# Optimization experiments

Measured on AMD Instinct MI355X. Metric: run time of the kernel, lower is better.

Reference implementation:

```python
import jax, jax.numpy as jnp
import numpy as np

N_NODES = 100000
N_EDGES = 1000000
IN_DIM = 64
HID_DIM = 64


def _gcn_conv(x, W, b, rows, cols, deg_inv_sqrt):
    # x: [N, Fin] -> [N, Fout]; rows/cols already include self-loops
    xw = x @ W                                   # [N, Fout]
    norm = deg_inv_sqrt[rows] * deg_inv_sqrt[cols]  # [E+N]
    msg = xw[cols] * norm[:, None]               # gather + scale, [E+N, Fout]
    out = jax.ops.segment_sum(msg, rows, num_segments=x.shape[0])  # scatter-add
    return out + b


def _prelu(x, a):
    return jnp.where(x >= 0, x, a * x)


def _encode(x, edge_index, perm, W1, b1, prelu_a, W2, b2):
    N = x.shape[0]
    loops = jnp.arange(N, dtype=edge_index.dtype)
    rows = jnp.concatenate([edge_index[0], loops])
    cols = jnp.concatenate([edge_index[1], loops])
    deg = jax.ops.segment_sum(jnp.ones_like(rows, dtype=x.dtype), rows, num_segments=N)
    dis = jnp.where(deg > 0, jax.lax.rsqrt(deg), 0.0)

    def enc(feat):
        h = _gcn_conv(feat, W1, b1, rows, cols, dis)
        h = _prelu(h, prelu_a)
        return _gcn_conv(h, W2, b2, rows, cols, dis)

    positive = enc(x)
    negative = enc(x[perm])  # corruption: row permutation of features
    summary = jax.nn.sigmoid(positive.mean(axis=0))
    return positive, negative, summary


def setup_inputs() -> dict:
    key = jax.random.key(0)
    kx, ke, kp, k1, k2 = jax.random.split(key, 5)
    x = jax.random.normal(kx, (N_NODES, IN_DIM), dtype=jnp.float32)
    edge_index = jax.random.randint(ke, (2, N_EDGES), 0, N_NODES, dtype=jnp.int32)
    perm = jax.random.permutation(kp, N_NODES).astype(jnp.int32)
    s1 = 1.0 / np.sqrt(IN_DIM)
    s2 = 1.0 / np.sqrt(HID_DIM)
    W1 = jax.random.uniform(k1, (IN_DIM, HID_DIM), jnp.float32, -s1, s1)
    b1 = jnp.zeros((HID_DIM,), jnp.float32)
    W2 = jax.random.uniform(k2, (HID_DIM, HID_DIM), jnp.float32, -s2, s2)
    b2 = jnp.zeros((HID_DIM,), jnp.float32)
    prelu_a = jnp.float32(0.25)
    return {"x": x, "edge_index": edge_index, "perm": perm,
            "W1": W1, "b1": b1, "prelu_a": prelu_a, "W2": W2, "b2": b2}


def reference(x, edge_index, perm, W1, b1, prelu_a, W2, b2):
    return _encode(x, edge_index, perm, W1, b1, prelu_a, W2, b2)
```

## Files before the change

kernel.cpp:

```cpp
#include <hip/hip_runtime.h>
#include <hip/hip_fp16.h>
#include <math.h>

namespace {

constexpr int NN = 100000;
constexpr int NE = 1000000;
constexpr int D  = 64;

constexpr int RPB_LOG = 8;
constexpr int RPB = 1 << RPB_LOG;
constexpr int NBUK = (NN + RPB - 1) >> RPB_LOG;
constexpr int CAP = 4096;
constexpr int TILE = 8192;
constexpr int NTILES = (NE + TILE - 1) / TILE;
constexpr int EPT = TILE / 512;
constexpr int G1B = (NN / 16 + 7) / 8;

using ushort_t = unsigned short;
typedef __attribute__((ext_vector_type(8))) short short8;
typedef __attribute__((ext_vector_type(4))) float f32x4;

union FragU { uint4 v; short8 s; };

__device__ inline void split2(float f0, float f1, unsigned int& hi, unsigned int& lo) {
    unsigned int u0 = __float_as_uint(f0);
    unsigned int u1 = __float_as_uint(f1);
    hi = (u0 >> 16) | (u1 & 0xffff0000u);
    float l0 = f0 - __uint_as_float(u0 & 0xffff0000u);
    float l1 = f1 - __uint_as_float(u1 & 0xffff0000u);
    lo = (__float_as_uint(l0) >> 16) | (__float_as_uint(l1) & 0xffff0000u);
}

__device__ inline unsigned int packh(float a, float b) {
    union { __half2 h; unsigned int u; } cv;
    cv.h = __float22half2_rn(make_float2(a, b));
    return cv.u;
}

__device__ inline float2 h2f(unsigned int v) {
    union { unsigned int u; __half2 h; } cv;
    cv.u = v;
    return __half22float2(cv.h);
}

__device__ inline void build_wfrags(const float* __restrict__ W, int lane,
                                    FragU (&whi)[4][2], FragU (&wlo)[4][2]) {
#pragma unroll
    for (int ft = 0; ft < 4; ++ft) {
#pragma unroll
        for (int kt = 0; kt < 2; ++kt) {
            int m  = ft * 16 + (lane & 15);
            int k0 = kt * 32 + (lane >> 4) * 8;
            unsigned int hi0, lo0, hi1, lo1, hi2, lo2, hi3, lo3;
            split2(W[(k0 + 0) * 64 + m], W[(k0 + 1) * 64 + m], hi0, lo0);
            split2(W[(k0 + 2) * 64 + m], W[(k0 + 3) * 64 + m], hi1, lo1);
            split2(W[(k0 + 4) * 64 + m], W[(k0 + 5) * 64 + m], hi2, lo2);
            split2(W[(k0 + 6) * 64 + m], W[(k0 + 7) * 64 + m], hi3, lo3);
            whi[ft][kt].v = make_uint4(hi0, hi1, hi2, hi3);
            wlo[ft][kt].v = make_uint4(lo0, lo1, lo2, lo3);
        }
    }
}

__global__ void pre_k(const int* __restrict__ rows, const int* __restrict__ cols,
                      int* __restrict__ bcount, unsigned int* __restrict__ binned, int e,
                      const float* __restrict__ W1, const float* __restrict__ W2,
                      uint4* __restrict__ fb,
                      const float* __restrict__ x, const int* __restrict__ perm,
                      ushort_t* __restrict__ tPN) {
    __shared__ int hist[NBUK];
    __shared__ int gbase[NBUK];
    __shared__ int lofs[NBUK];
    int bid = blockIdx.x;

    if (bid > NTILES) {
        int lane  = threadIdx.x & 63;
        int wtile = (bid - NTILES - 1) * 8 + (threadIdx.x >> 6);
        if (wtile * 16 >= NN) return;
        int node = wtile * 16 + (lane & 15);
        int kg   = lane >> 4;

        FragU whi[4][2];
        FragU wlo[4][2];
        build_wfrags(W1, lane, whi, wlo);

        const float4* xr = (const float4*)x;
        size_t rbase = (size_t)node * 16 + (size_t)(kg * 2);
        int pnode = perm[node];
        size_t pbase = (size_t)pnode * 16 + (size_t)(kg * 2);
        f32x4 accP[4];
        f32x4 accN[4];
#pragma unroll
        for (int ft = 0; ft < 4; ++ft) {
            accP[ft] = f32x4{0.f, 0.f, 0.f, 0.f};
            accN[ft] = f32x4{0.f, 0.f, 0.f, 0.f};
        }
#pragma unroll
        for (int kt = 0; kt < 2; ++kt) {
            float4 a0 = xr[rbase + kt * 8];
            float4 a1 = xr[rbase + kt * 8 + 1];
            float4 g0 = xr[pbase + kt * 8];
            float4 g1 = xr[pbase + kt * 8 + 1];
            unsigned int h0, l0, h1, l1, h2, l2, h3, l3;
            split2(a0.x, a0.y, h0, l0);
            split2(a0.z, a0.w, h1, l1);
            split2(a1.x, a1.y, h2, l2);
            split2(a1.z, a1.w, h3, l3);
            FragU xhiP, xloP;
            xhiP.v = make_uint4(h0, h1, h2, h3);
            xloP.v = make_uint4(l0, l1, l2, l3);
            split2(g0.x, g0.y, h0, l0);
            split2(g0.z, g0.w, h1, l1);
            split2(g1.x, g1.y, h2, l2);
            split2(g1.z, g1.w, h3, l3);
            FragU xhiN, xloN;
            xhiN.v = make_uint4(h0, h1, h2, h3);
            xloN.v = make_uint4(l0, l1, l2, l3);
#pragma unroll
            for (int ft = 0; ft < 4; ++ft) {
                accP[ft] = __builtin_amdgcn_mfma_f32_16x16x32_bf16(whi[ft][kt].s, xhiP.s, accP[ft], 0, 0, 0);
                accP[ft] = __builtin_amdgcn_mfma_f32_16x16x32_bf16(whi[ft][kt].s, xloP.s, accP[ft], 0, 0, 0);
                accP[ft] = __builtin_amdgcn_mfma_f32_16x16x32_bf16(wlo[ft][kt].s, xhiP.s, accP[ft], 0, 0, 0);
                accN[ft] = __builtin_amdgcn_mfma_f32_16x16x32_bf16(whi[ft][kt].s, xhiN.s, accN[ft], 0, 0, 0);
                accN[ft] = __builtin_amdgcn_mfma_f32_16x16x32_bf16(whi[ft][kt].s, xloN.s, accN[ft], 0, 0, 0);
                accN[ft] = __builtin_amdgcn_mfma_f32_16x16x32_bf16(wlo[ft][kt].s, xhiN.s, accN[ft], 0, 0, 0);
            }
        }
        int fo = kg * 4;
        ushort_t* p = tPN + (size_t)node * 128;
#pragma unroll
        for (int ft = 0; ft < 4; ++ft) {
            uint2 up = make_uint2(packh(accP[ft][0], accP[ft][1]),
                                  packh(accP[ft][2], accP[ft][3]));
            *(uint2*)(p + ft * 16 + fo) = up;
            uint2 un = make_uint2(packh(accN[ft][0], accN[ft][1]),
                                  packh(accN[ft][2], accN[ft][3]));
            *(uint2*)(p + 64 + ft * 16 + fo) = un;
        }
        return;
    }

    if (bid == NTILES) {
        int lane = threadIdx.x;
        if (lane < 64) {
            for (int ft = 0; ft < 4; ++ft) {
                for (int kt = 0; kt < 2; ++kt) {
                    int m  = ft * 16 + (lane & 15);
                    int k0 = kt * 32 + (lane >> 4) * 8;
                    unsigned int hi0, lo0, hi1, lo1, hi2, lo2, hi3, lo3;
                    split2(W2[(k0 + 0) * 64 + m], W2[(k0 + 1) * 64 + m], hi0, lo0);
                    split2(W2[(k0 + 2) * 64 + m], W2[(k0 + 3) * 64 + m], hi1, lo1);
                    split2(W2[(k0 + 4) * 64 + m], W2[(k0 + 5) * 64 + m], hi2, lo2);
                    split2(W2[(k0 + 6) * 64 + m], W2[(k0 + 7) * 64 + m], hi3, lo3);
                    fb[((ft * 2 + kt) * 2 + 0) * 64 + lane] = make_uint4(hi0, hi1, hi2, hi3);
                    fb[((ft * 2 + kt) * 2 + 1) * 64 + lane] = make_uint4(lo0, lo1, lo2, lo3);
                }
            }
        }
        return;
    }

    int base = bid * TILE;
    for (int i = threadIdx.x; i < NBUK; i += blockDim.x) {
        hist[i] = 0;
        lofs[i] = 0;
    }
    __syncthreads();
    int r[EPT];
    int c[EPT];
    int bk[EPT];
#pragma unroll
    for (int j = 0; j < EPT; ++j) {
        int i = base + j * 512 + (int)threadIdx.x;
        if (i < e) {
            r[j] = rows[i];
            c[j] = cols[i];
            bk[j] = r[j] >> RPB_LOG;
            atomicAdd(&hist[bk[j]], 1);
        } else {
            bk[j] = -1;
        }
    }
    __syncthreads();
    for (int b = threadIdx.x; b < NBUK; b += blockDim.x) {
        int h = hist[b];
        gbase[b] = h ? atomicAdd(&bcount[b], h) : 0;
    }
    __syncthreads();
#pragma unroll
    for (int j = 0; j < EPT; ++j) {
        if (bk[j] >= 0) {
            int l = gbase[bk[j]] + atomicAdd(&lofs[bk[j]], 1);
            if (l < CAP) {
                unsigned int v = ((unsigned int)(r[j] & (RPB - 1)) << 17) | (unsigned int)c[j];
                binned[(size_t)bk[j] * CAP + l] = v;
            }
        }
    }
}

__global__ void bucket_sort_k(const unsigned int* __restrict__ binned,
                              const int* __restrict__ bcount,
                              int* __restrict__ scols, int* __restrict__ rowstart,
                              int* __restrict__ deg, float* __restrict__ dis) {
    __shared__ int lcur[RPB];
    __shared__ int srs[RPB];
    __shared__ int wsum[8];
    __shared__ int redpart[8];
    __shared__ int sbase;
    int b = blockIdx.x;
    int row0 = b << RPB_LOG;
    int nrows = min(RPB, NN - row0);
    int cnt = bcount[b];
    const unsigned int* src = binned + (size_t)b * CAP;
    int tid = threadIdx.x;
    int lane = tid & 63;
    int wid = tid >> 6;

    int bv = (tid < NBUK && tid < b) ? bcount[tid] : 0;
    int bs = bv;
#pragma unroll
    for (int off = 1; off < 64; off <<= 1) {
        bs += __shfl_xor(bs, off, 64);
    }
    if (lane == 0) redpart[wid] = bs;
    __syncthreads();
    if (tid == 0) {
        int t = 0;
        for (int w = 0; w < 8; ++w) t += redpart[w];
        sbase = t;
    }
    if (tid < RPB) {
        lcur[tid] = 0;
    }
    __syncthreads();
    int bb = sbase;

    for (int i = tid; i < cnt; i += blockDim.x) {
        atomicAdd(&lcur[src[i] >> 17], 1);
    }
    __syncthreads();
    int d = (tid < nrows) ? lcur[tid] : 0;
    int inc = d;
#pragma unroll
    for (int off = 1; off < 64; off <<= 1) {
        int t = __shfl_up(inc, off);
        if (lane >= off) inc += t;
    }
    if (lane == 63) wsum[wid] = inc;
    __syncthreads();
    int wpre = 0;
    for (int w = 0; w < wid; ++w) wpre += wsum[w];
    int gstart = bb + wpre + inc - d;
    if (tid < nrows) {
        rowstart[row0 + tid] = gstart;
        deg[row0 + tid] = d;
        dis[row0 + tid] = rsqrtf((float)(d + 1));
    }
    __syncthreads();
    if (tid < RPB) {
        srs[tid] = gstart;
        lcur[tid] = 0;
    }
    __syncthreads();
    for (int i = tid; i < cnt; i += blockDim.x) {
        unsigned int v = src[i];
        int rl = (int)(v >> 17);
        int pos = srs[rl] + atomicAdd(&lcur[rl], 1);
        scols[pos] = (int)(v & 0x1FFFFu);
    }
}

__global__ void agg_gemm_k(const ushort_t* __restrict__ tIn, ushort_t* __restrict__ tOut,
                           const float* __restrict__ dis,
                           const int* __restrict__ rowstart, const int* __restrict__ deg,
                           const int* __restrict__ scols,
                           const float* __restrict__ bias, const float* __restrict__ prelu_a,
                           const uint4* __restrict__ wf) {
    __shared__ float Hs[2][16][68];
    int tid = threadIdx.x;
    int lane = tid & 63;
    int wv = tid >> 6;
    int row0 = blockIdx.x * 16;
    int hl = lane & 31;
    int half = lane >> 5;
    size_t lofs = (size_t)(half * 64 + hl * 2);
    float aPr = *prelu_a;

    for (int rr = 0; rr < 4; ++rr) {
        int r = row0 + wv * 4 + rr;
        int rs   = __builtin_amdgcn_readfirstlane(r);
        int base = __builtin_amdgcn_readfirstlane(rowstart[rs]);
        int dg   = __builtin_amdgcn_readfirstlane(deg[rs]);
        float dr = dis[rs];
        unsigned int sv = *(const unsigned int*)(tIn + (size_t)rs * 128 + lofs);
        float2 fs = h2f(sv);
        float a0 = dr * fs.x;
        float a1 = dr * fs.y;
        int j = 0;
        for (; j + 4 <= dg; j += 4) {
            int c0 = scols[base + j];
            int c1 = scols[base + j + 1];
            int c2 = scols[base + j + 2];
            int c3 = scols[base + j + 3];
            float d0 = dis[c0];
            float d1 = dis[c1];
            float d2 = dis[c2];
            float d3 = dis[c3];
            unsigned int v0 = *(const unsigned int*)(tIn + (size_t)c0 * 128 + lofs);
            unsigned int v1 = *(const unsigned int*)(tIn + (size_t)c1 * 128 + lofs);
            unsigned int v2 = *(const unsigned int*)(tIn + (size_t)c2 * 128 + lofs);
            unsigned int v3 = *(const unsigned int*)(tIn + (size_t)c3 * 128 + lofs);
            float2 f0 = h2f(v0);
            float2 f1 = h2f(v1);
            float2 f2 = h2f(v2);
            float2 f3 = h2f(v3);
            a0 = fmaf(d0, f0.x, a0);
            a1 = fmaf(d0, f0.y, a1);
            a0 = fmaf(d1, f1.x, a0);
            a1 = fmaf(d1, f1.y, a1);
            a0 = fmaf(d2, f2.x, a0);
            a1 = fmaf(d2, f2.y, a1);
            a0 = fmaf(d3, f3.x, a0);
            a1 = fmaf(d3, f3.y, a1);
        }
        for (; j < dg; ++j) {
            int c = scols[base + j];
            float dc = dis[c];
            unsigned int v = *(const unsigned int*)(tIn + (size_t)c * 128 + lofs);
            float2 f = h2f(v);
            a0 = fmaf(dc, f.x, a0);
            a1 = fmaf(dc, f.y, a1);
        }
        float2 bv = *(const float2*)(bias + 2 * hl);
        float v0 = fmaf(dr, a0, bv.x);
        float v1 = fmaf(dr, a1, bv.y);
        v0 = v0 >= 0.f ? v0 : aPr * v0;
        v1 = v1 >= 0.f ? v1 : aPr * v1;
        int rl = wv * 4 + rr;
        Hs[half][rl][2 * hl]     = v0;
        Hs[half][rl][2 * hl + 1] = v1;
    }
    __syncthreads();

    int kg = lane >> 4;
    int nd = lane & 15;
    int hsel = wv >> 1;
    int ftb = (wv & 1) * 2;
    FragU whi[2][2];
    FragU wlo[2][2];
#pragma unroll
    for (int f2 = 0; f2 < 2; ++f2) {
#pragma unroll
        for (int kt = 0; kt < 2; ++kt) {
            whi[f2][kt].v = wf[(((ftb + f2) * 2 + kt) * 2 + 0) * 64 + lane];
            wlo[f2][kt].v = wf[(((ftb + f2) * 2 + kt) * 2 + 1) * 64 + lane];
        }
    }
    f32x4 acc[2];
    acc[0] = f32x4{0.f, 0.f, 0.f, 0.f};
    acc[1] = f32x4{0.f, 0.f, 0.f, 0.f};
#pragma unroll
    for (int kt = 0; kt < 2; ++kt) {
        float4 a0 = *(const float4*)&Hs[hsel][nd][kt * 32 + kg * 8];
        float4 a1 = *(const float4*)&Hs[hsel][nd][kt * 32 + kg * 8 + 4];
        unsigned int h0, l0, h1, l1, h2, l2, h3, l3;
        split2(a0.x, a0.y, h0, l0);
        split2(a0.z, a0.w, h1, l1);
        split2(a1.x, a1.y, h2, l2);
        split2(a1.z, a1.w, h3, l3);
        FragU xhi, xlo;
        xhi.v = make_uint4(h0, h1, h2, h3);
        xlo.v = make_uint4(l0, l1, l2, l3);
#pragma unroll
        for (int f2 = 0; f2 < 2; ++f2) {
            acc[f2] = __builtin_amdgcn_mfma_f32_16x16x32_bf16(whi[f2][kt].s, xhi.s, acc[f2], 0, 0, 0);
            acc[f2] = __builtin_amdgcn_mfma_f32_16x16x32_bf16(whi[f2][kt].s, xlo.s, acc[f2], 0, 0, 0);
            acc[f2] = __builtin_amdgcn_mfma_f32_16x16x32_bf16(wlo[f2][kt].s, xhi.s, acc[f2], 0, 0, 0);
        }
    }
    float s = dis[row0 + nd];
    ushort_t* p = tOut + (size_t)(row0 + nd) * 128 + hsel * 64;
    int fo = kg * 4;
#pragma unroll
    for (int f2 = 0; f2 < 2; ++f2) {
        uint2 u = make_uint2(packh(s * acc[f2][0], s * acc[f2][1]),
                             packh(s * acc[f2][2], s * acc[f2][3]));
        *(uint2*)(p + (ftb + f2) * 16 + fo) = u;
    }
}

__global__ void agg_dual_k(const ushort_t* __restrict__ tPN,
                           float* __restrict__ dstP, float* __restrict__ dstN,
                           const float* __restrict__ dis,
                           const int* __restrict__ rowstart, const int* __restrict__ deg,
                           const int* __restrict__ scols,
                           const float* __restrict__ bias, int n) {
    int lane = threadIdx.x & 63;
    int hl = lane & 31;
    int half = lane >> 5;
    int r = blockIdx.x * (blockDim.x >> 6) + (threadIdx.x >> 6);
    if (r >= n) return;
    int rs   = __builtin_amdgcn_readfirstlane(r);
    int base = __builtin_amdgcn_readfirstlane(rowstart[rs]);
    int dg   = __builtin_amdgcn_readfirstlane(deg[rs]);
    float dr = dis[rs];
    size_t lofs = (size_t)(half * 64 + hl * 2);
    unsigned int sv = *(const unsigned int*)(tPN + (size_t)rs * 128 + lofs);
    float2 fs = h2f(sv);
    float a0 = fs.x;
    float a1 = fs.y;
    int j = 0;
    for (; j + 4 <= dg; j += 4) {
        int c0 = scols[base + j];
        int c1 = scols[base + j + 1];
        int c2 = scols[base + j + 2];
        int c3 = scols[base + j + 3];
        unsigned int v0 = *(const unsigned int*)(tPN + (size_t)c0 * 128 + lofs);
        unsigned int v1 = *(const unsigned int*)(tPN + (size_t)c1 * 128 + lofs);
        unsigned int v2 = *(const unsigned int*)(tPN + (size_t)c2 * 128 + lofs);
        unsigned int v3 = *(const unsigned int*)(tPN + (size_t)c3 * 128 + lofs);
        float2 f0 = h2f(v0);
        float2 f1 = h2f(v1);
        float2 f2 = h2f(v2);
        float2 f3 = h2f(v3);
        a0 += f0.x + f1.x + f2.x + f3.x;
        a1 += f0.y + f1.y + f2.y + f3.y;
    }
    for (; j < dg; ++j) {
        int c = scols[base + j];
        unsigned int v = *(const unsigned int*)(tPN + (size_t)c * 128 + lofs);
        float2 f = h2f(v);
        a0 += f.x;
        a1 += f.y;
    }
    float2 bv = *(const float2*)(bias + 2 * hl);
    float v0 = fmaf(dr, a0, bv.x);
    float v1 = fmaf(dr, a1, bv.y);
    float* dst = half ? dstN : dstP;
    *(float2*)(dst + (size_t)rs * D + 2 * hl) = float2{v0, v1};
}

__global__ void summary_partial_k(const float* __restrict__ pos, float* __restrict__ acc, int n) {
    __shared__ float red[4][64];
    int lane = threadIdx.x & 63;
    int wv = threadIdx.x >> 6;
    int wave = (blockIdx.x * blockDim.x + threadIdx.x) >> 6;
    int nw = (gridDim.x * blockDim.x) >> 6;
    float s0 = 0.f, s1 = 0.f, s2 = 0.f, s3 = 0.f;
    int r = wave;
    for (; r + 3 * nw < n; r += 4 * nw) {
        s0 += pos[(size_t)r * D + lane];
        s1 += pos[(size_t)(r + nw) * D + lane];
        s2 += pos[(size_t)(r + 2 * nw) * D + lane];
        s3 += pos[(size_t)(r + 3 * nw) * D + lane];
    }
    for (; r < n; r += nw) {
        s0 += pos[(size_t)r * D + lane];
    }
    red[wv][lane] = (s0 + s1) + (s2 + s3);
    __syncthreads();
    if (wv == 0) {
        float t = (red[0][lane] + red[1][lane]) + (red[2][lane] + red[3][lane]);
        atomicAdd(&acc[lane], t);
    }
}

__global__ void summary_final_k(const float* __restrict__ acc, float* __restrict__ out, int n) {
    int f = threadIdx.x;
    if (f < D) {
        float m = acc[f] / (float)n;
        out[f] = 1.f / (1.f + expf(-m));
    }
}

}

extern "C" void kernel_launch(void* const* d_in, const int* in_sizes, int n_in,
                              void* d_out, int out_size, void* d_ws, size_t ws_size,
                              hipStream_t stream) {
    (void)in_sizes; (void)n_in; (void)out_size; (void)ws_size;
    const float* x       = (const float*)d_in[0];
    const int*   ei      = (const int*)  d_in[1];
    const int*   perm    = (const int*)  d_in[2];
    const float* W1      = (const float*)d_in[3];
    const float* b1      = (const float*)d_in[4];
    const float* prelu_a = (const float*)d_in[5];
    const float* W2      = (const float*)d_in[6];
    const float* b2      = (const float*)d_in[7];

    float* outP = (float*)d_out;
    float* outN = outP + (size_t)NN * D;
    float* outS = outN + (size_t)NN * D;

    const int* erows = ei;
    const int* ecols = ei + NE;

    char* ws = (char*)d_ws;
    size_t off = 0;
    auto alloc = [&](size_t bytes) {
        void* p = ws + off;
        off = (off + bytes + 255) & ~(size_t)255;
        return p;
    };
    int*      deg      = (int*)     alloc((size_t)NN * 4);
    float*    dis      = (float*)   alloc((size_t)NN * 4);
    int*      rowstart = (int*)     alloc((size_t)NN * 4);
    int*      bcount   = (int*)     alloc((size_t)NBUK * 4);
    float*    acc      = (float*)   alloc((size_t)D * 4);
    unsigned int* binned = (unsigned int*)alloc((size_t)NBUK * CAP * 4);
    int*      scols    = (int*)     alloc((size_t)NE * 4);
    ushort_t* tPN      = (ushort_t*)alloc((size_t)NN * 128 * 2);
    ushort_t* tPN2     = (ushort_t*)alloc((size_t)NN * 128 * 2);
    uint4*    wfrag    = (uint4*)   alloc((size_t)1024 * 16);

    hipMemsetAsync(bcount, 0, (size_t)((char*)acc - (char*)bcount) + (size_t)D * 4, stream);

    pre_k<<<NTILES + 1 + G1B, 512, 0, stream>>>(erows, ecols, bcount, binned, NE,
                                                W1, W2, wfrag, x, perm, tPN);
    bucket_sort_k<<<NBUK, 512, 0, stream>>>(binned, bcount, scols, rowstart, deg, dis);

    agg_gemm_k<<<NN / 16, 256, 0, stream>>>(tPN, tPN2, dis, rowstart, deg, scols,
                                            b1, prelu_a, wfrag);

    agg_dual_k<<<(NN + 3) / 4, 256, 0, stream>>>(tPN2, outP, outN, dis, rowstart, deg,
                                                 scols, b2, NN);

    summary_partial_k<<<512, 256, 0, stream>>>(outP, acc, NN);
    summary_final_k<<<1, 64, 0, stream>>>(acc, outS, NN);
}
```

Baseline: 241.3 us.

## Fuse summary reduction into final aggregation and simplify binning histogram

The column-sum for the summary is now computed inside the final aggregation kernel and accumulated into 256 striped partial buffers via atomics, which removes the separate pass that re-read the positive output. The edge binning kernel uses a single shared-memory atomic per edge to get both the histogram count and the local slot, dropping the second atomic pass. W2 fragment splitting moves from a dedicated block into each agg_gemm block, which removes one block and a global buffer at the cost of redundant per-block work. Striped atomics reduce contention, and a small final kernel sums the partial buffers.

```diff
diff --git a/kernel.cpp b/kernel.cpp
--- a/kernel.cpp
+++ b/kernel.cpp
@@ -16,6 +16,7 @@
 constexpr int NTILES = (NE + TILE - 1) / TILE;
 constexpr int EPT = TILE / 512;
 constexpr int G1B = (NN / 16 + 7) / 8;
+constexpr int SUMS = 256;
 
 using ushort_t = unsigned short;
 typedef __attribute__((ext_vector_type(8))) short short8;
@@ -65,18 +66,16 @@
 
 __global__ void pre_k(const int* __restrict__ rows, const int* __restrict__ cols,
                       int* __restrict__ bcount, unsigned int* __restrict__ binned, int e,
-                      const float* __restrict__ W1, const float* __restrict__ W2,
-                      uint4* __restrict__ fb,
+                      const float* __restrict__ W1,
                       const float* __restrict__ x, const int* __restrict__ perm,
                       ushort_t* __restrict__ tPN) {
-    __shared__ int hist[NBUK];
     __shared__ int gbase[NBUK];
     __shared__ int lofs[NBUK];
     int bid = blockIdx.x;
 
-    if (bid > NTILES) {
+    if (bid >= NTILES) {
         int lane  = threadIdx.x & 63;
-        int wtile = (bid - NTILES - 1) * 8 + (threadIdx.x >> 6);
+        int wtile = (bid - NTILES) * 8 + (threadIdx.x >> 6);
         if (wtile * 16 >= NN) return;
         int node = wtile * 16 + (lane & 15);
         int kg   = lane >> 4;
@@ -141,60 +140,39 @@
         return;
     }
 
-    if (bid == NTILES) {
-        int lane = threadIdx.x;
-        if (lane < 64) {
-            for (int ft = 0; ft < 4; ++ft) {
-                for (int kt = 0; kt < 2; ++kt) {
-                    int m  = ft * 16 + (lane & 15);
-                    int k0 = kt * 32 + (lane >> 4) * 8;
-                    unsigned int hi0, lo0, hi1, lo1, hi2, lo2, hi3, lo3;
-                    split2(W2[(k0 + 0) * 64 + m], W2[(k0 + 1) * 64 + m], hi0, lo0);
-                    split2(W2[(k0 + 2) * 64 + m], W2[(k0 + 3) * 64 + m], hi1, lo1);
-                    split2(W2[(k0 + 4) * 64 + m], W2[(k0 + 5) * 64 + m], hi2, lo2);
-                    split2(W2[(k0 + 6) * 64 + m], W2[(k0 + 7) * 64 + m], hi3, lo3);
-                    fb[((ft * 2 + kt) * 2 + 0) * 64 + lane] = make_uint4(hi0, hi1, hi2, hi3);
-                    fb[((ft * 2 + kt) * 2 + 1) * 64 + lane] = make_uint4(lo0, lo1, lo2, lo3);
-                }
-            }
-        }
-        return;
-    }
-
     int base = bid * TILE;
     for (int i = threadIdx.x; i < NBUK; i += blockDim.x) {
-        hist[i] = 0;
         lofs[i] = 0;
     }
     __syncthreads();
-    int r[EPT];
-    int c[EPT];
+    unsigned int v[EPT];
     int bk[EPT];
+    int lx[EPT];
 #pragma unroll
     for (int j = 0; j < EPT; ++j) {
         int i = base + j * 512 + (int)threadIdx.x;
         if (i < e) {
-            r[j] = rows[i];
-            c[j] = cols[i];
-            bk[j] = r[j] >> RPB_LOG;
-            atomicAdd(&hist[bk[j]], 1);
+            int r = rows[i];
+            int c = cols[i];
+            bk[j] = r >> RPB_LOG;
+            v[j] = ((unsigned int)(r & (RPB - 1)) << 17) | (unsigned int)c;
+            lx[j] = atomicAdd(&lofs[bk[j]], 1);
         } else {
             bk[j] = -1;
         }
     }
     __syncthreads();
     for (int b = threadIdx.x; b < NBUK; b += blockDim.x) {
-        int h = hist[b];
+        int h = lofs[b];
         gbase[b] = h ? atomicAdd(&bcount[b], h) : 0;
     }
     __syncthreads();
 #pragma unroll
     for (int j = 0; j < EPT; ++j) {
         if (bk[j] >= 0) {
-            int l = gbase[bk[j]] + atomicAdd(&lofs[bk[j]], 1);
-            if (l < CAP) {
-                unsigned int v = ((unsigned int)(r[j] & (RPB - 1)) << 17) | (unsigned int)c[j];
-                binned[(size_t)bk[j] * CAP + l] = v;
+            int p = gbase[bk[j]] + lx[j];
+            if (p < CAP) {
+                binned[(size_t)bk[j] * CAP + p] = v[j];
             }
         }
     }
@@ -277,7 +255,7 @@
                            const int* __restrict__ rowstart, const int* __restrict__ deg,
                            const int* __restrict__ scols,
                            const float* __restrict__ bias, const float* __restrict__ prelu_a,
-                           const uint4* __restrict__ wf) {
+                           const float* __restrict__ W2) {
     __shared__ float Hs[2][16][68];
     int tid = threadIdx.x;
     int lane = tid & 63;
@@ -354,8 +332,15 @@
     for (int f2 = 0; f2 < 2; ++f2) {
 #pragma unroll
         for (int kt = 0; kt < 2; ++kt) {
-            whi[f2][kt].v = wf[(((ftb + f2) * 2 + kt) * 2 + 0) * 64 + lane];
-            wlo[f2][kt].v = wf[(((ftb + f2) * 2 + kt) * 2 + 1) * 64 + lane];
+            int m  = (ftb + f2) * 16 + (lane & 15);
+            int k0 = kt * 32 + (lane >> 4) * 8;
+            unsigned int hi0, lo0, hi1, lo1, hi2, lo2, hi3, lo3;
+            split2(W2[(k0 + 0) * 64 + m], W2[(k0 + 1) * 64 + m], hi0, lo0);
+            split2(W2[(k0 + 2) * 64 + m], W2[(k0 + 3) * 64 + m], hi1, lo1);
+            split2(W2[(k0 + 4) * 64 + m], W2[(k0 + 5) * 64 + m], hi2, lo2);
+            split2(W2[(k0 + 6) * 64 + m], W2[(k0 + 7) * 64 + m], hi3, lo3);
+            whi[f2][kt].v = make_uint4(hi0, hi1, hi2, hi3);
+            wlo[f2][kt].v = make_uint4(lo0, lo1, lo2, lo3);
         }
     }
     f32x4 acc[2];
@@ -396,81 +381,81 @@
                            const float* __restrict__ dis,
                            const int* __restrict__ rowstart, const int* __restrict__ deg,
                            const int* __restrict__ scols,
-                           const float* __restrict__ bias, int n) {
+                           const float* __restrict__ bias,
+                           float* __restrict__ acc2, int n) {
+    __shared__ float red[4][64];
     int lane = threadIdx.x & 63;
     int hl = lane & 31;
     int half = lane >> 5;
-    int r = blockIdx.x * (blockDim.x >> 6) + (threadIdx.x >> 6);
-    if (r >= n) return;
-    int rs   = __builtin_amdgcn_readfirstlane(r);
-    int base = __builtin_amdgcn_readfirstlane(rowstart[rs]);
-    int dg   = __builtin_amdgcn_readfirstlane(deg[rs]);
-    float dr = dis[rs];
-    size_t lofs = (size_t)(half * 64 + hl * 2);
-    unsigned int sv = *(const unsigned int*)(tPN + (size_t)rs * 128 + lofs);
-    float2 fs = h2f(sv);
-    float a0 = fs.x;
-    float a1 = fs.y;
-    int j = 0;
-    for (; j + 4 <= dg; j += 4) {
-        int c0 = scols[base + j];
-        int c1 = scols[base + j + 1];
-        int c2 = scols[base + j + 2];
-        int c3 = scols[base + j + 3];
-        unsigned int v0 = *(const unsigned int*)(tPN + (size_t)c0 * 128 + lofs);
-        unsigned int v1 = *(const unsigned int*)(tPN + (size_t)c1 * 128 + lofs);
-        unsigned int v2 = *(const unsigned int*)(tPN + (size_t)c2 * 128 + lofs);
-        unsigned int v3 = *(const unsigned int*)(tPN + (size_t)c3 * 128 + lofs);
-        float2 f0 = h2f(v0);
-        float2 f1 = h2f(v1);
-        float2 f2 = h2f(v2);
-        float2 f3 = h2f(v3);
-        a0 += f0.x + f1.x + f2.x + f3.x;
-        a1 += f0.y + f1.y + f2.y + f3.y;
-    }
-    for (; j < dg; ++j) {
-        int c = scols[base + j];
-        unsigned int v = *(const unsigned int*)(tPN + (size_t)c * 128 + lofs);
-        float2 f = h2f(v);
-        a0 += f.x;
-        a1 += f.y;
-    }
-    float2 bv = *(const float2*)(bias + 2 * hl);
-    float v0 = fmaf(dr, a0, bv.x);
-    float v1 = fmaf(dr, a1, bv.y);
-    float* dst = half ? dstN : dstP;
-    *(float2*)(dst + (size_t)rs * D + 2 * hl) = float2{v0, v1};
-}
-
-__global__ void summary_partial_k(const float* __restrict__ pos, float* __restrict__ acc, int n) {
+    int wv = threadIdx.x >> 6;
+    int r = blockIdx.x * (blockDim.x >> 6) + wv;
+    float v0 = 0.f;
+    float v1 = 0.f;
+    if (r < n) {
+        int rs   = __builtin_amdgcn_readfirstlane(r);
+        int base = __builtin_amdgcn_readfirstlane(rowstart[rs]);
+        int dg   = __builtin_amdgcn_readfirstlane(deg[rs]);
+        float dr = dis[rs];
+        size_t lofs = (size_t)(half * 64 + hl * 2);
+        unsigned int sv = *(const unsigned int*)(tPN + (size_t)rs * 128 + lofs);
+        float2 fs = h2f(sv);
+        float a0 = fs.x;
+        float a1 = fs.y;
+        int j = 0;
+        for (; j + 4 <= dg; j += 4) {
+            int c0 = scols[base + j];
+            int c1 = scols[base + j + 1];
+            int c2 = scols[base + j + 2];
+            int c3 = scols[base + j + 3];
+            unsigned int u0 = *(const unsigned int*)(tPN + (size_t)c0 * 128 + lofs);
+            unsigned int u1 = *(const unsigned int*)(tPN + (size_t)c1 * 128 + lofs);
+            unsigned int u2 = *(const unsigned int*)(tPN + (size_t)c2 * 128 + lofs);
+            unsigned int u3 = *(const unsigned int*)(tPN + (size_t)c3 * 128 + lofs);
+            float2 f0 = h2f(u0);
+            float2 f1 = h2f(u1);
+            float2 f2 = h2f(u2);
+            float2 f3 = h2f(u3);
+            a0 += f0.x + f1.x + f2.x + f3.x;
+            a1 += f0.y + f1.y + f2.y + f3.y;
+        }
+        for (; j < dg; ++j) {
+            int c = scols[base + j];
+            unsigned int u = *(const unsigned int*)(tPN + (size_t)c * 128 + lofs);
+            float2 f = h2f(u);
+            a0 += f.x;
+            a1 += f.y;
+        }
+        float2 bv = *(const float2*)(bias + 2 * hl);
+        v0 = fmaf(dr, a0, bv.x);
+        v1 = fmaf(dr, a1, bv.y);
+        float* dst = half ? dstN : dstP;
+        *(float2*)(dst + (size_t)rs * D + 2 * hl) = float2{v0, v1};
+    }
+    if (half == 0) {
+        red[wv][2 * hl]     = v0;
+        red[wv][2 * hl + 1] = v1;
+    }
+    __syncthreads();
+    if (threadIdx.x < 64) {
+        float t = (red[0][threadIdx.x] + red[1][threadIdx.x]) +
+                  (red[2][threadIdx.x] + red[3][threadIdx.x]);
+        atomicAdd(&acc2[((blockIdx.x & (SUMS - 1)) << 6) + threadIdx.x], t);
+    }
+}
+
+__global__ void summary_final_k(const float* __restrict__ acc2, float* __restrict__ out, int n) {
     __shared__ float red[4][64];
-    int lane = threadIdx.x & 63;
-    int wv = threadIdx.x >> 6;
-    int wave = (blockIdx.x * blockDim.x + threadIdx.x) >> 6;
-    int nw = (gridDim.x * blockDim.x) >> 6;
-    float s0 = 0.f, s1 = 0.f, s2 = 0.f, s3 = 0.f;
-    int r = wave;
-    for (; r + 3 * nw < n; r += 4 * nw) {
-        s0 += pos[(size_t)r * D + lane];
-        s1 += pos[(size_t)(r + nw) * D + lane];
-        s2 += pos[(size_t)(r + 2 * nw) * D + lane];
-        s3 += pos[(size_t)(r + 3 * nw) * D + lane];
-    }
-    for (; r < n; r += nw) {
-        s0 += pos[(size_t)r * D + lane];
-    }
-    red[wv][lane] = (s0 + s1) + (s2 + s3);
-    __syncthreads();
-    if (wv == 0) {
-        float t = (red[0][lane] + red[1][lane]) + (red[2][lane] + red[3][lane]);
-        atomicAdd(&acc[lane], t);
-    }
-}
-
-__global__ void summary_final_k(const float* __restrict__ acc, float* __restrict__ out, int n) {
-    int f = threadIdx.x;
-    if (f < D) {
-        float m = acc[f] / (float)n;
+    int f = threadIdx.x & 63;
+    int g = threadIdx.x >> 6;
+    float t = 0.f;
+#pragma unroll
+    for (int k = 0; k < SUMS / 4; ++k) {
+        t += acc2[((g + 4 * k) << 6) + f];
+    }
+    red[g][f] = t;
+    __syncthreads();
+    if (threadIdx.x < 64) {
+        float m = (red[0][f] + red[1][f] + red[2][f] + red[3][f]) / (float)n;
         out[f] = 1.f / (1.f + expf(-m));
     }
 }
@@ -508,25 +493,24 @@
     float*    dis      = (float*)   alloc((size_t)NN * 4);
     int*      rowstart = (int*)     alloc((size_t)NN * 4);
     int*      bcount   = (int*)     alloc((size_t)NBUK * 4);
-    float*    acc      = (float*)   alloc((size_t)D * 4);
+    float*    acc2     = (float*)   alloc((size_t)SUMS * D * 4);
     unsigned int* binned = (unsigned int*)alloc((size_t)NBUK * CAP * 4);
     int*      scols    = (int*)     alloc((size_t)NE * 4);
     ushort_t* tPN      = (ushort_t*)alloc((size_t)NN * 128 * 2);
     ushort_t* tPN2     = (ushort_t*)alloc((size_t)NN * 128 * 2);
-    uint4*    wfrag    = (uint4*)   alloc((size_t)1024 * 16);
-
-    hipMemsetAsync(bcount, 0, (size_t)((char*)acc - (char*)bcount) + (size_t)D * 4, stream);
-
-    pre_k<<<NTILES + 1 + G1B, 512, 0, stream>>>(erows, ecols, bcount, binned, NE,
-                                                W1, W2, wfrag, x, perm, tPN);
+
+    hipMemsetAsync(bcount, 0,
+                   (size_t)((char*)acc2 - (char*)bcount) + (size_t)SUMS * D * 4, stream);
+
+    pre_k<<<NTILES + G1B, 512, 0, stream>>>(erows, ecols, bcount, binned, NE,
+                                            W1, x, perm, tPN);
     bucket_sort_k<<<NBUK, 512, 0, stream>>>(binned, bcount, scols, rowstart, deg, dis);
 
     agg_gemm_k<<<NN / 16, 256, 0, stream>>>(tPN, tPN2, dis, rowstart, deg, scols,
-                                            b1, prelu_a, wfrag);
+                                            b1, prelu_a, W2);
 
     agg_dual_k<<<(NN + 3) / 4, 256, 0, stream>>>(tPN2, outP, outN, dis, rowstart, deg,
-                                                 scols, b2, NN);
-
-    summary_partial_k<<<512, 256, 0, stream>>>(outP, acc, NN);
-    summary_final_k<<<1, 64, 0, stream>>>(acc, outS, NN);
-}
+                                                 scols, b2, acc2, NN);
+
+    summary_final_k<<<1, 256, 0, stream>>>(acc2, outS, NN);
+}
```

New measurement: 232.5 us. -3.7%, faster.
